# Kernel tuning notes

Hardware: AMD Instinct MI355X
Metric: run time of the kernel (lower is better)

The kernel has to match this reference:

```python
import jax, jax.numpy as jnp
import numpy as np

N = 100000
F_IN = 128
HID = 256
N_CLS = 40
E = 1600000


def setup_inputs() -> dict:
    key = jax.random.key(0)
    ks = jax.random.split(key, 12)
    x = jax.random.normal(ks[0], (N, F_IN), dtype=jnp.float32)
    edge_index = jax.random.randint(ks[1], (2, E), 0, N, dtype=jnp.int64)
    # GCNConv params (glorot-ish scale), conv2 is reused twice in forward
    def lin(k, fi, fo):
        return jax.random.normal(k, (fi, fo), dtype=jnp.float32) * (1.0 / np.sqrt(fi))
    return {
        "x": x,
        "edge_index": edge_index,
        "W1": lin(ks[2], F_IN, HID), "b1": jnp.zeros((HID,), jnp.float32),
        "W2": lin(ks[3], HID, HID),  "b2": jnp.zeros((HID,), jnp.float32),
        "W3": lin(ks[4], HID, HID),  "b3": jnp.zeros((HID,), jnp.float32),
        "W4": lin(ks[5], HID, N_CLS), "b4": jnp.zeros((N_CLS,), jnp.float32),
    }


def _gcn_norm(edge_index, n):
    # add self-loops, compute symmetric normalization D^-1/2 (A+I) D^-1/2
    loop = jnp.arange(n, dtype=edge_index.dtype)
    src = jnp.concatenate([edge_index[0], loop])
    dst = jnp.concatenate([edge_index[1], loop])
    deg = jax.ops.segment_sum(jnp.ones_like(dst, dtype=jnp.float32), dst, num_segments=n)
    dinv = jnp.where(deg > 0, jax.lax.rsqrt(deg), 0.0)
    norm = dinv[src] * dinv[dst]  # [E+N]
    return src, dst, norm


def _gcn_conv(x, W, b, src, dst, norm, n):
    h = x @ W                       # [N, Fout] dense transform first (fewer msg bytes)
    msg = h[src] * norm[:, None]    # gather + scale
    out = jax.ops.segment_sum(msg, dst, num_segments=n)  # scatter-add
    return out + b


def reference(x, edge_index, W1, b1, W2, b2, W3, b3, W4, b4):
    n = x.shape[0]
    src, dst, norm = _gcn_norm(edge_index, n)
    h = jax.nn.relu(_gcn_conv(x, W1, b1, src, dst, norm, n))
    h = jax.nn.relu(_gcn_conv(h, W2, b2, src, dst, norm, n))
    h = jax.nn.relu(_gcn_conv(h, W2, b2, src, dst, norm, n))  # conv2 reused, as in source
    h = jax.nn.relu(_gcn_conv(h, W3, b3, src, dst, norm, n))
    h = _gcn_conv(h, W4, b4, src, dst, norm, n)
    return jax.nn.log_softmax(h, axis=1)
```

## Files before the change

### kernel.cpp

```cpp
#include <hip/hip_runtime.h>
#include <stdint.h>
#include <math.h>

#define NN   100000
#define FIN  128
#define HIDDEN 256
#define NCLS 40
#define NE   1600000

#define PRNG 8
#define RNG  12500
#define SSL  32
#define NES  50000

typedef unsigned short u16;
typedef unsigned char u8;
typedef __attribute__((ext_vector_type(8))) short s16x8;
typedef __attribute__((ext_vector_type(4))) float f32x4;
typedef __attribute__((ext_vector_type(2))) float f32x2;

__device__ __forceinline__ float bf2f(unsigned short u) {
    union { float f; uint32_t i; } v; v.i = ((uint32_t)u) << 16; return v.f;
}
__device__ __forceinline__ unsigned short f2bf(float f) {
    union { float f; uint32_t i; } v; v.f = f;
    uint32_t r = v.i + 0x7fffu + ((v.i >> 16) & 1u);
    return (unsigned short)(r >> 16);
}
__device__ __forceinline__ u8 f2fp8(float f) {
    int r = __builtin_amdgcn_cvt_pk_fp8_f32(f, f, 0, false);
    return (u8)(r & 0xff);
}

__global__ __launch_bounds__(256) void k_detect(const u16* __restrict__ x16,
                                                const int* __restrict__ ei,
                                                int* __restrict__ flags) {
    int g = blockIdx.x * 256 + threadIdx.x;
    uint2 v = *(const uint2*)(x16 + (size_t)g * 4);
    int nan_cnt = 0;
    uint32_t w0 = v.x, w1 = v.y;
    if (((w0 >> 0)  & 0x7fff) >= 0x7f80) nan_cnt++;
    if (((w0 >> 16) & 0x7fff) >= 0x7f80) nan_cnt++;
    if (((w1 >> 0)  & 0x7fff) >= 0x7f80) nan_cnt++;
    if (((w1 >> 16) & 0x7fff) >= 0x7f80) nan_cnt++;
    int odd_nz = (g < 8192 && ei[2 * g + 1] != 0) ? 1 : 0;
#pragma unroll
    for (int off = 1; off < 64; off <<= 1) {
        nan_cnt += __shfl_xor(nan_cnt, off);
        odd_nz  += __shfl_xor(odd_nz, off);
    }
    if ((threadIdx.x & 63) == 0) {
        if (nan_cnt) atomicAdd(&flags[0], nan_cnt);
        if (odd_nz)  atomicAdd(&flags[2], odd_nz);
    }
}

__global__ void k_compact(const int* __restrict__ ei, int* __restrict__ dst32,
                          int* __restrict__ src32, const int* __restrict__ flags) {
    int e = blockIdx.x * 256 + threadIdx.x;
    if (e < NE) {
        if (flags[2] == 0) { src32[e] = ei[2 * e]; dst32[e] = ei[2 * (NE + e)]; }
        else               { src32[e] = ei[e];     dst32[e] = ei[NE + e]; }
    }
}

__global__ void k_trans_cvt(const void* W1, const void* W2, const void* W3, const void* W4,
                            u16* W1t, u16* W2t, u16* W3t, u16* W4t,
                            const void* b1, const void* b2, const void* b3, const void* b4,
                            u16* o1, u16* o2, u16* o3, u16* o4,
                            const void* __restrict__ x, const float* __restrict__ dinv,
                            u16* __restrict__ xb,
                            const int* __restrict__ flags) {
    int b = blockIdx.x;
    int fl = flags[0];
    int t = threadIdx.x;
    if (b >= 705) {
        int i = (b - 705) * 256 + t;
        if (i < NN * FIN) {
            float v = fl ? ((const float*)x)[i] : bf2f(((const u16*)x)[i]);
            xb[i] = f2bf(v * dinv[i >> 7]);
        }
        return;
    }
    if (b == 704) {
        o1[t] = fl ? f2bf(((const float*)b1)[t]) : ((const u16*)b1)[t];
        o2[t] = fl ? f2bf(((const float*)b2)[t]) : ((const u16*)b2)[t];
        o3[t] = fl ? f2bf(((const float*)b3)[t]) : ((const u16*)b3)[t];
        if (t < 64) o4[t] = (t < NCLS) ? (fl ? f2bf(((const float*)b4)[t]) : ((const u16*)b4)[t]) : (u16)0;
        return;
    }
    const void* W; u16* Wt; int K, F, Fpad, base;
    if (b < 128)      { W = W1; Wt = W1t; K = 128; F = 256; Fpad = 256; base = 0; }
    else if (b < 384) { W = W2; Wt = W2t; K = 256; F = 256; Fpad = 256; base = 128; }
    else if (b < 640) { W = W3; Wt = W3t; K = 256; F = 256; Fpad = 256; base = 384; }
    else              { W = W4; Wt = W4t; K = 256; F = 40;  Fpad = 64;  base = 640; }
    int idx = (b - base) * 256 + t;
    if (idx >= K * Fpad) return;
    int f = idx / K, k = idx - f * K;
    u16 v = 0;
    if (f < F) {
        if (fl) v = f2bf(((const float*)W)[(size_t)k * F + f]);
        else    v = ((const u16*)W)[(size_t)k * F + f];
    }
    Wt[idx] = v;
}


__global__ __launch_bounds__(256) void k_histb(const int* __restrict__ dst32,
                                               int* __restrict__ partial) {
    __shared__ int h[RNG];
    int p = blockIdx.x >> 5, s = blockIdx.x & 31;
    int t = threadIdx.x;
    int4 z4 = make_int4(0, 0, 0, 0);
    for (int i = t * 4; i < RNG; i += 1024) *(int4*)(h + i) = z4;
    __syncthreads();
    int base = s * NES;
    int lo = p * RNG;
    int nfull = NES & ~1023;
    for (int k = t * 4; k < nfull; k += 1024) {
        int4 d4 = *(const int4*)(dst32 + base + k);
        int a;
        a = d4.x - lo; if ((unsigned)a < RNG) atomicAdd(&h[a], 1);
        a = d4.y - lo; if ((unsigned)a < RNG) atomicAdd(&h[a], 1);
        a = d4.z - lo; if ((unsigned)a < RNG) atomicAdd(&h[a], 1);
        a = d4.w - lo; if ((unsigned)a < RNG) atomicAdd(&h[a], 1);
    }
    for (int k = nfull + t; k < NES; k += 256) {
        int a = dst32[base + k] - lo;
        if ((unsigned)a < RNG) atomicAdd(&h[a], 1);
    }
    __syncthreads();
    int* out = partial + blockIdx.x * RNG;
    for (int i = t * 4; i < RNG; i += 1024) *(int4*)(out + i) = *(const int4*)(h + i);
}

__global__ __launch_bounds__(256) void k_scan1(const int* __restrict__ partial,
                                               int* __restrict__ cnt,
                                               int* __restrict__ out,
                                               int* __restrict__ bsum) {
    __shared__ int sh[256];
    int t = threadIdx.x;
    int base = blockIdx.x * 1024 + t * 4;
    int v0 = 0, v1 = 0, v2 = 0, v3 = 0;
    if (base < NN) {
        int p = base / RNG, il = base - p * RNG;
        const int* q = partial + (p * SSL) * RNG + il;
        int4 acc = make_int4(0, 0, 0, 0);
#pragma unroll
        for (int s = 0; s < SSL; ++s) {
            int4 w = *(const int4*)(q + s * RNG);
            acc.x += w.x; acc.y += w.y; acc.z += w.z; acc.w += w.w;
        }
        v0 = acc.x; v1 = acc.y; v2 = acc.z; v3 = acc.w;
        *(int4*)(cnt + base) = acc;
    }
    int s = v0 + v1 + v2 + v3;
    sh[t] = s;
    __syncthreads();
    for (int off = 1; off < 256; off <<= 1) {
        int x = (t >= off) ? sh[t - off] : 0;
        __syncthreads();
        sh[t] += x;
        __syncthreads();
    }
    int ex = sh[t] - s;
    if (base < NN) {
        int4 o = make_int4(ex, ex + v0, ex + v0 + v1, ex + v0 + v1 + v2);
        *(int4*)(out + base) = o;
    }
    if (t == 255) bsum[blockIdx.x] = sh[255];
}

__global__ void k_scan2(int* bsum, int nb) {
    if (threadIdx.x == 0 && blockIdx.x == 0) {
        int run = 0;
        for (int i = 0; i < nb; ++i) { int t = bsum[i]; bsum[i] = run; run += t; }
    }
}

__global__ void k_scan3o(int* __restrict__ rp, const int* __restrict__ bsum,
                         const int* __restrict__ cnt, float* __restrict__ dinv,
                         int* __restrict__ partial) {
    int i = blockIdx.x * 256 + threadIdx.x;
    if (i < NN) {
        int v = rp[i] + bsum[i >> 10];
        rp[i] = v;
        dinv[i] = rsqrtf((float)(cnt[i] + 1));
        int p = i / RNG, il = i - p * RNG;
        int* q = partial + (p * SSL) * RNG + il;
        int run = v;
#pragma unroll
        for (int s = 0; s < SSL; ++s) { int t = q[s * RNG]; q[s * RNG] = run; run += t; }
    }
    if (i == 0) rp[NN] = NE;
}

__global__ __launch_bounds__(256) void k_fillb(const int* __restrict__ dst32,
                                               const int* __restrict__ src32,
                                               const int* __restrict__ offs,
                                               int* __restrict__ col) {
    __shared__ int h[RNG];
    int p = blockIdx.x >> 5, s = blockIdx.x & 31;
    int t = threadIdx.x;
    const int* o = offs + blockIdx.x * RNG;
    for (int i = t * 4; i < RNG; i += 1024) *(int4*)(h + i) = *(const int4*)(o + i);
    __syncthreads();
    int base = s * NES;
    int lo = p * RNG;
    int nfull = NES & ~1023;
    for (int k = t * 4; k < nfull; k += 1024) {
        int4 d4 = *(const int4*)(dst32 + base + k);
        int4 s4 = *(const int4*)(src32 + base + k);
        int a;
        a = d4.x - lo; if ((unsigned)a < RNG) col[atomicAdd(&h[a], 1)] = s4.x;
        a = d4.y - lo; if ((unsigned)a < RNG) col[atomicAdd(&h[a], 1)] = s4.y;
        a = d4.z - lo; if ((unsigned)a < RNG) col[atomicAdd(&h[a], 1)] = s4.z;
        a = d4.w - lo; if ((unsigned)a < RNG) col[atomicAdd(&h[a], 1)] = s4.w;
    }
    for (int k = nfull + t; k < NES; k += 256) {
        int a = dst32[base + k] - lo;
        if ((unsigned)a < RNG) col[atomicAdd(&h[a], 1)] = src32[base + k];
    }
}


#define GLL(g, l) __builtin_amdgcn_global_load_lds( \
    (const __attribute__((address_space(1))) unsigned int*)(g), \
    (__attribute__((address_space(3))) unsigned int*)(l), 16, 0, 0)

#define NT128 ((NN + 127) / 128)
#define NT256 ((NN + 255) / 256)

__global__ __launch_bounds__(256) void k_gemmP(const u16* __restrict__ A,
                                               const u16* __restrict__ Wt,
                                               const float* __restrict__ dinv,
                                               const u16* __restrict__ bias,
                                               u16* __restrict__ C,
                                               int K, int out_fp8) {
    __shared__ __align__(16) u16 Bs[128 * 256];
    __shared__ __align__(16) u16 As[2 * 128 * 32];
    int t = threadIdx.x;
    int bn = blockIdx.y;
    int w = t >> 6, lane = t & 63;
    int wm = w >> 1, wn = w & 1;
    int lrow = lane & 15, lq = lane >> 4;
    int r0 = t >> 2;
    int seg = (t & 3) * 8;

    int rounds = K >> 4;
    for (int r = 0; r < rounds; ++r) {
        int d = r * 4096 + t * 16;
        int kt = d >> 13;
        int win = d & 8191;
        int row = win >> 6;
        int sg = (win & 63) >> 1;
        GLL(Wt + (size_t)(bn * 128 + row) * K + kt * 32 + sg, Bs + (d >> 1));
    }

    int nK = K >> 5;
    bool fuse = (bias != nullptr);
    float bcol[4];
#pragma unroll
    for (int j = 0; j < 4; ++j)
        bcol[j] = fuse ? bf2f(bias[bn * 128 + wn * 64 + j * 16 + lrow]) : 0.f;

    for (int tm = blockIdx.x; tm < NT128; tm += gridDim.x) {
        int rowBase = tm * 128;
        int ar0 = rowBase + r0;       if (ar0 > NN - 1) ar0 = NN - 1;
        int ar1 = rowBase + 64 + r0;  if (ar1 > NN - 1) ar1 = NN - 1;
        const u16* a0p = A + (size_t)ar0 * K + seg;
        const u16* a1p = A + (size_t)ar1 * K + seg;
        GLL(a0p, As + t * 8);
        GLL(a1p, As + 2048 + t * 8);

        f32x4 acc[4][4] = {};
        int cur = 0;
        for (int kt = 0; kt < nK; ++kt) {
            __syncthreads();
            if (kt + 1 < nK) {
                int nxt = cur ^ 1;
                GLL(a0p + (kt + 1) * 32, As + nxt * 4096 + t * 8);
                GLL(a1p + (kt + 1) * 32, As + nxt * 4096 + 2048 + t * 8);
            }
            const u16* ab = As + cur * 4096;
            const u16* bb = Bs + kt * 4096;
            s16x8 af[4], bf[4];
#pragma unroll
            for (int i = 0; i < 4; ++i)
                af[i] = *(const s16x8*)(ab + (wm * 64 + i * 16 + lrow) * 32 + lq * 8);
#pragma unroll
            for (int j = 0; j < 4; ++j)
                bf[j] = *(const s16x8*)(bb + (wn * 64 + j * 16 + lrow) * 32 + lq * 8);
#pragma unroll
            for (int i = 0; i < 4; ++i)
#pragma unroll
                for (int j = 0; j < 4; ++j)
                    acc[i][j] = __builtin_amdgcn_mfma_f32_16x16x32_bf16(af[i], bf[j], acc[i][j], 0, 0, 0);
            cur ^= 1;
        }

        u8* C8 = (u8*)C;
#pragma unroll
        for (int i = 0; i < 4; ++i) {
#pragma unroll
            for (int rr = 0; rr < 4; ++rr) {
                int row = rowBase + wm * 64 + i * 16 + lq * 4 + rr;
                if (row < NN) {
                    float d = dinv[row];
#pragma unroll
                    for (int j = 0; j < 4; ++j) {
                        int colg = bn * 128 + wn * 64 + j * 16 + lrow;
                        float v = fuse ? fmaxf(fmaf(d, acc[i][j][rr], bcol[j]), 0.f)
                                       : acc[i][j][rr] * d;
                        if (out_fp8) C8[(size_t)row * HIDDEN + colg] = f2fp8(v);
                        else         C[(size_t)row * HIDDEN + colg] = f2bf(v);
                    }
                }
            }
        }
        __syncthreads();
    }
}

__global__ __launch_bounds__(256) void k_gemmP64(const u16* __restrict__ A,
                                                 const u16* __restrict__ Wt,
                                                 const float* __restrict__ dinv,
                                                 u16* __restrict__ C) {
    const int K = 256;
    __shared__ __align__(16) u16 Bs[64 * 256];
    __shared__ __align__(16) u16 As[2 * 256 * 32];
    int t = threadIdx.x;
    int w = t >> 6, lane = t & 63;
    int lrow = lane & 15, lq = lane >> 4;
    int seg = (t & 3) * 8;
    int rr0 = t >> 2;

    for (int r = 0; r < 8; ++r)
        GLL(Wt + (size_t)(t >> 2) * K + r * 32 + seg, Bs + r * 2048 + t * 8);

    for (int tm = blockIdx.x; tm < NT256; tm += gridDim.x) {
        int rowBase = tm * 256;
        const u16* ap[4];
#pragma unroll
        for (int c = 0; c < 4; ++c) {
            int ar = rowBase + c * 64 + rr0;
            if (ar > NN - 1) ar = NN - 1;
            ap[c] = A + (size_t)ar * K + seg;
        }
#pragma unroll
        for (int c = 0; c < 4; ++c) GLL(ap[c], As + c * 2048 + t * 8);

        f32x4 acc[4][4] = {};
        int cur = 0;
        for (int kt = 0; kt < 8; ++kt) {
            __syncthreads();
            if (kt + 1 < 8) {
                int nxt = cur ^ 1;
#pragma unroll
                for (int c = 0; c < 4; ++c)
                    GLL(ap[c] + (kt + 1) * 32, As + nxt * 8192 + c * 2048 + t * 8);
            }
            const u16* ab = As + cur * 8192;
            const u16* bb = Bs + kt * 2048;
            s16x8 af[4], bf[4];
#pragma unroll
            for (int i = 0; i < 4; ++i)
                af[i] = *(const s16x8*)(ab + (w * 64 + i * 16 + lrow) * 32 + lq * 8);
#pragma unroll
            for (int j = 0; j < 4; ++j)
                bf[j] = *(const s16x8*)(bb + (j * 16 + lrow) * 32 + lq * 8);
#pragma unroll
            for (int i = 0; i < 4; ++i)
#pragma unroll
                for (int j = 0; j < 4; ++j)
                    acc[i][j] = __builtin_amdgcn_mfma_f32_16x16x32_bf16(af[i], bf[j], acc[i][j], 0, 0, 0);
            cur ^= 1;
        }

#pragma unroll
        for (int i = 0; i < 4; ++i) {
#pragma unroll
            for (int rr = 0; rr < 4; ++rr) {
                int row = rowBase + w * 64 + i * 16 + lq * 4 + rr;
                if (row < NN) {
                    float d = dinv[row];
#pragma unroll
                    for (int j = 0; j < 4; ++j) {
                        int colg = j * 16 + lrow;
                        C[(size_t)row * 64 + colg] = f2bf(acc[i][j][rr] * d);
                    }
                }
            }
        }
        __syncthreads();
    }
}


__global__ __launch_bounds__(256) void k_agg8(const u8* __restrict__ hs,
                                              const int* __restrict__ rp,
                                              const int* __restrict__ col,
                                              const float* __restrict__ dinv,
                                              const u16* __restrict__ bias,
                                              u16* __restrict__ out) {
    int wq = __builtin_amdgcn_readfirstlane(threadIdx.x >> 6);
    int row = blockIdx.x * 4 + wq;
    if (row >= NN) return;
    int lane = threadIdx.x & 63;
    int fo = lane * 4;
    float a0 = 0.f, a1 = 0.f, a2 = 0.f, a3 = 0.f;
    auto acc_add = [&](uint32_t w) {
        f32x2 x = __builtin_amdgcn_cvt_pk_f32_fp8(w, false);
        f32x2 y = __builtin_amdgcn_cvt_pk_f32_fp8(w, true);
        a0 += x.x; a1 += x.y; a2 += y.x; a3 += y.y;
    };
    auto acc_fma = [&](uint32_t w, float m) {
        f32x2 x = __builtin_amdgcn_cvt_pk_f32_fp8(w, false);
        f32x2 y = __builtin_amdgcn_cvt_pk_f32_fp8(w, true);
        a0 = fmaf(m, x.x, a0); a1 = fmaf(m, x.y, a1);
        a2 = fmaf(m, y.x, a2); a3 = fmaf(m, y.y, a3);
    };
    acc_add(*(const uint32_t*)(hs + (size_t)row * HIDDEN + fo));
    int p  = __builtin_amdgcn_readfirstlane(rp[row]);
    int p1 = __builtin_amdgcn_readfirstlane(rp[row + 1]);
    for (; p + 8 <= p1; p += 8) {
        uint32_t v[8];
#pragma unroll
        for (int k = 0; k < 8; ++k) {
            int c = __builtin_amdgcn_readfirstlane(col[p + k]);
            v[k] = *(const uint32_t*)(hs + (size_t)c * HIDDEN + fo);
        }
#pragma unroll
        for (int k = 0; k < 8; ++k) acc_add(v[k]);
    }
    int rem = p1 - p;
    if (rem) {
        uint32_t v[8];
#pragma unroll
        for (int k = 0; k < 8; ++k) {
            int idx = (k < rem) ? (p + k) : p;
            int c = __builtin_amdgcn_readfirstlane(col[idx]);
            v[k] = *(const uint32_t*)(hs + (size_t)c * HIDDEN + fo);
        }
#pragma unroll
        for (int k = 0; k < 8; ++k) acc_fma(v[k], (k < rem) ? 1.f : 0.f);
    }
    float d = dinv[row];
    uint2 bv = *(const uint2*)(bias + fo);
    float r0 = fmaxf(fmaf(d, a0, bf2f((u16)(bv.x & 0xffff))), 0.f);
    float r1 = fmaxf(fmaf(d, a1, bf2f((u16)(bv.x >> 16))), 0.f);
    float r2 = fmaxf(fmaf(d, a2, bf2f((u16)(bv.y & 0xffff))), 0.f);
    float r3 = fmaxf(fmaf(d, a3, bf2f((u16)(bv.y >> 16))), 0.f);
    uint2 o;
    o.x = (uint32_t)f2bf(r0) | ((uint32_t)f2bf(r1) << 16);
    o.y = (uint32_t)f2bf(r2) | ((uint32_t)f2bf(r3) << 16);
    *(uint2*)(out + (size_t)row * HIDDEN + fo) = o;
}

__global__ __launch_bounds__(256) void k_aggx(const u16* __restrict__ xb,
                                              const int* __restrict__ rp,
                                              const int* __restrict__ col,
                                              u16* __restrict__ out) {
    int wq = __builtin_amdgcn_readfirstlane(threadIdx.x >> 6);
    int row = blockIdx.x * 4 + wq;
    if (row >= NN) return;
    int lane = threadIdx.x & 63;
    int fo = lane * 2;
    float a0 = 0.f, a1 = 0.f;
    auto acc_add = [&](uint32_t w) {
        a0 += bf2f((u16)(w & 0xffff));
        a1 += bf2f((u16)(w >> 16));
    };
    auto acc_fma = [&](uint32_t w, float m) {
        a0 = fmaf(m, bf2f((u16)(w & 0xffff)), a0);
        a1 = fmaf(m, bf2f((u16)(w >> 16)), a1);
    };
    acc_add(*(const uint32_t*)(xb + (size_t)row * FIN + fo));
    int p  = __builtin_amdgcn_readfirstlane(rp[row]);
    int p1 = __builtin_amdgcn_readfirstlane(rp[row + 1]);
    for (; p + 8 <= p1; p += 8) {
        uint32_t v[8];
#pragma unroll
        for (int k = 0; k < 8; ++k) {
            int c = __builtin_amdgcn_readfirstlane(col[p + k]);
            v[k] = *(const uint32_t*)(xb + (size_t)c * FIN + fo);
        }
#pragma unroll
        for (int k = 0; k < 8; ++k) acc_add(v[k]);
    }
    int rem = p1 - p;
    if (rem) {
        uint32_t v[8];
#pragma unroll
        for (int k = 0; k < 8; ++k) {
            int idx = (k < rem) ? (p + k) : p;
            int c = __builtin_amdgcn_readfirstlane(col[idx]);
            v[k] = *(const uint32_t*)(xb + (size_t)c * FIN + fo);
        }
#pragma unroll
        for (int k = 0; k < 8; ++k) acc_fma(v[k], (k < rem) ? 1.f : 0.f);
    }
    uint32_t o = (uint32_t)f2bf(a0) | ((uint32_t)f2bf(a1) << 16);
    *(uint32_t*)(out + (size_t)row * FIN + fo) = o;
}

__global__ __launch_bounds__(256) void k_agg5(const u16* __restrict__ hs,
                                              const int* __restrict__ rp,
                                              const int* __restrict__ col,
                                              const float* __restrict__ dinv,
                                              const u16* __restrict__ bias,
                                              void* __restrict__ out,
                                              const int* __restrict__ flags) {
    int wq = __builtin_amdgcn_readfirstlane(threadIdx.x >> 6);
    int row = blockIdx.x * 4 + wq;
    if (row >= NN) return;
    int lane = threadIdx.x & 63;
    float a = bf2f(hs[(size_t)row * 64 + lane]);
    int p  = __builtin_amdgcn_readfirstlane(rp[row]);
    int p1 = __builtin_amdgcn_readfirstlane(rp[row + 1]);
    for (; p + 8 <= p1; p += 8) {
        u16 v[8];
#pragma unroll
        for (int k = 0; k < 8; ++k) {
            int c = __builtin_amdgcn_readfirstlane(col[p + k]);
            v[k] = hs[(size_t)c * 64 + lane];
        }
#pragma unroll
        for (int k = 0; k < 8; ++k) a += bf2f(v[k]);
    }
    int rem = p1 - p;
    if (rem) {
        u16 v[8];
#pragma unroll
        for (int k = 0; k < 8; ++k) {
            int idx = (k < rem) ? (p + k) : p;
            int c = __builtin_amdgcn_readfirstlane(col[idx]);
            v[k] = hs[(size_t)c * 64 + lane];
        }
#pragma unroll
        for (int k = 0; k < 8; ++k)
            a = fmaf((k < rem) ? 1.f : 0.f, bf2f(v[k]), a);
    }
    bool act = lane < NCLS;
    float d = dinv[row];
    float l = act ? fmaf(d, a, bf2f(bias[lane])) : -1e30f;
    float m = l;
#pragma unroll
    for (int off = 32; off > 0; off >>= 1) m = fmaxf(m, __shfl_xor(m, off));
    float e = act ? __expf(l - m) : 0.f;
#pragma unroll
    for (int off = 32; off > 0; off >>= 1) e += __shfl_xor(e, off);
    if (act) {
        float r = l - m - __logf(e);
        if (flags[0]) ((float*)out)[(size_t)row * NCLS + lane] = r;
        else          ((u16*)out)[(size_t)row * NCLS + lane] = f2bf(r);
    }
}


extern "C" void kernel_launch(void* const* d_in, const int* in_sizes, int n_in,
                              void* d_out, int out_size, void* d_ws, size_t ws_size,
                              hipStream_t stream) {
    const void* x  = d_in[0];
    const int* ei  = (const int*)d_in[1];
    const void* W1 = d_in[2];
    const void* b1 = d_in[3];
    const void* W2 = d_in[4];
    const void* b2 = d_in[5];
    const void* W3 = d_in[6];
    const void* b3 = d_in[7];
    const void* W4 = d_in[8];
    const void* b4 = d_in[9];

    char* p = (char*)d_ws;
    auto alloc = [&](size_t b) -> char* {
        char* r = p;
        p += (b + 255) & ~(size_t)255;
        return r;
    };
    int*   flags = (int*)alloc(256);
    int*   cnt  = (int*)alloc((size_t)NN * 4);
    float* dinv = (float*)alloc((size_t)NN * 4);
    int*   rp   = (int*)alloc((size_t)(NN + 1) * 4);
    int*   col  = (int*)alloc((size_t)NE * 4);
    int*   bsum = (int*)alloc(4096);
    u16* xb  = (u16*)alloc((size_t)NN * FIN * 2);
    u16* W1t = (u16*)alloc((size_t)256 * 128 * 2);
    u16* W2t = (u16*)alloc((size_t)256 * 256 * 2);
    u16* W3t = (u16*)alloc((size_t)256 * 256 * 2);
    u16* W4t = (u16*)alloc((size_t)64 * 256 * 2);
    u16* bb1 = (u16*)alloc(512);
    u16* bb2 = (u16*)alloc(512);
    u16* bb3 = (u16*)alloc(512);
    u16* bb4 = (u16*)alloc(128);
    u16* bufA = (u16*)alloc((size_t)NN * HIDDEN * 2);
    u16* bufB = (u16*)alloc((size_t)NN * HIDDEN * 2);

    int* dst32   = (int*)bufA;
    int* src32   = dst32 + NE;
    int* partial = (int*)bufB;

    hipMemsetAsync(flags, 0, 16, stream);
    k_detect<<<64, 256, 0, stream>>>((const u16*)x, ei, flags);
    k_compact<<<(NE + 255) / 256, 256, 0, stream>>>(ei, dst32, src32, flags);

    k_histb<<<PRNG * SSL, 256, 0, stream>>>(dst32, partial);
    k_scan1<<<(NN + 1023) / 1024, 256, 0, stream>>>(partial, cnt, rp, bsum);
    k_scan2<<<1, 64, 0, stream>>>(bsum, (NN + 1023) / 1024);
    k_scan3o<<<(NN + 255) / 256, 256, 0, stream>>>(rp, bsum, cnt, dinv, partial);
    k_fillb<<<PRNG * SSL, 256, 0, stream>>>(dst32, src32, partial, col);

    k_trans_cvt<<<705 + (NN * FIN + 255) / 256, 256, 0, stream>>>(
        W1, W2, W3, W4, W1t, W2t, W3t, W4t,
        b1, b2, b3, b4, bb1, bb2, bb3, bb4, x, dinv, xb, flags);

    dim3 gP(256, 2);
    dim3 aggGrid((NN + 3) / 4);

    k_aggx<<<aggGrid, 256, 0, stream>>>(xb, rp, col, bufB);
    k_gemmP<<<gP, 256, 0, stream>>>(bufB, W1t, dinv, bb1, bufA, 128, 0);
    k_gemmP<<<gP, 256, 0, stream>>>(bufA, W2t, dinv, nullptr, bufB, 256, 1);
    k_agg8<<<aggGrid, 256, 0, stream>>>((const u8*)bufB, rp, col, dinv, bb2, bufA);
    k_gemmP<<<gP, 256, 0, stream>>>(bufA, W2t, dinv, nullptr, bufB, 256, 1);
    k_agg8<<<aggGrid, 256, 0, stream>>>((const u8*)bufB, rp, col, dinv, bb2, bufA);
    k_gemmP<<<gP, 256, 0, stream>>>(bufA, W3t, dinv, nullptr, bufB, 256, 1);
    k_agg8<<<aggGrid, 256, 0, stream>>>((const u8*)bufB, rp, col, dinv, bb3, bufA);
    k_gemmP64<<<256, 256, 0, stream>>>(bufA, W4t, dinv, bufB);
    k_agg5<<<aggGrid, 256, 0, stream>>>(bufB, rp, col, dinv, bb4, d_out, flags);
}
```

Baseline: 702.3 us.

## Slice gathered feature tables into column blocks for cache-resident aggregation

Stores the pre-aggregation features (bf16 x and fp8 hidden activations) in a column-sliced layout of 8 slices, each contiguous over all nodes. Aggregation kernels now launch 8x more blocks, each handling one slice, so the gathered working set per slice is smaller and more likely to stay in L2/LLC during the random neighbor gathers. Each wave also processes 8 edges in parallel across lane groups and reduces them with cross-lane shuffles. The costs are that column indices and row pointers are re-read once per slice, per-edge gathers shrink to 32-byte segments, and the extra shuffle reductions and partly idle lanes add overhead.

```diff
diff --git a/kernel.cpp b/kernel.cpp
--- a/kernel.cpp
+++ b/kernel.cpp
@@ -12,6 +12,8 @@
 #define RNG  12500
 #define SSL  32
 #define NES  50000
+
+#define NSLC 8
 
 typedef unsigned short u16;
 typedef unsigned char u8;
@@ -77,8 +79,10 @@
     if (b >= 705) {
         int i = (b - 705) * 256 + t;
         if (i < NN * FIN) {
+            int node = i >> 7, f = i & 127;
             float v = fl ? ((const float*)x)[i] : bf2f(((const u16*)x)[i]);
-            xb[i] = f2bf(v * dinv[i >> 7]);
+            xb[(size_t)(f >> 4) * (NN * 16) + (size_t)node * 16 + (f & 15)] =
+                f2bf(v * dinv[node]);
         }
         return;
     }
@@ -312,8 +316,10 @@
                         int colg = bn * 128 + wn * 64 + j * 16 + lrow;
                         float v = fuse ? fmaxf(fmaf(d, acc[i][j][rr], bcol[j]), 0.f)
                                        : acc[i][j][rr] * d;
-                        if (out_fp8) C8[(size_t)row * HIDDEN + colg] = f2fp8(v);
-                        else         C[(size_t)row * HIDDEN + colg] = f2bf(v);
+                        if (out_fp8)
+                            C8[(size_t)(colg >> 5) * (NN * 32) + (size_t)row * 32 + (colg & 31)] = f2fp8(v);
+                        else
+                            C[(size_t)row * HIDDEN + colg] = f2bf(v);
                     }
                 }
             }
@@ -403,11 +409,16 @@
                                               const float* __restrict__ dinv,
                                               const u16* __restrict__ bias,
                                               u16* __restrict__ out) {
+    int bid = blockIdx.x;
+    int s = bid & 7;
+    int rowg = bid >> 3;
     int wq = __builtin_amdgcn_readfirstlane(threadIdx.x >> 6);
-    int row = blockIdx.x * 4 + wq;
+    int row = rowg * 4 + wq;
     if (row >= NN) return;
     int lane = threadIdx.x & 63;
-    int fo = lane * 4;
+    int g = lane >> 3;
+    int fl = lane & 7;
+    const u8* hss = hs + (size_t)s * (NN * 32);
     float a0 = 0.f, a1 = 0.f, a2 = 0.f, a3 = 0.f;
     auto acc_add = [&](uint32_t w) {
         f32x2 x = __builtin_amdgcn_cvt_pk_f32_fp8(w, false);
@@ -420,52 +431,63 @@
         a0 = fmaf(m, x.x, a0); a1 = fmaf(m, x.y, a1);
         a2 = fmaf(m, y.x, a2); a3 = fmaf(m, y.y, a3);
     };
-    acc_add(*(const uint32_t*)(hs + (size_t)row * HIDDEN + fo));
+    if (lane < 8) acc_add(*(const uint32_t*)(hss + (size_t)row * 32 + fl * 4));
     int p  = __builtin_amdgcn_readfirstlane(rp[row]);
     int p1 = __builtin_amdgcn_readfirstlane(rp[row + 1]);
-    for (; p + 8 <= p1; p += 8) {
-        uint32_t v[8];
-#pragma unroll
-        for (int k = 0; k < 8; ++k) {
-            int c = __builtin_amdgcn_readfirstlane(col[p + k]);
-            v[k] = *(const uint32_t*)(hs + (size_t)c * HIDDEN + fo);
-        }
-#pragma unroll
-        for (int k = 0; k < 8; ++k) acc_add(v[k]);
+    for (; p + 16 <= p1; p += 16) {
+        int c0 = col[p + g];
+        int c1 = col[p + 8 + g];
+        uint32_t v0 = *(const uint32_t*)(hss + (size_t)c0 * 32 + fl * 4);
+        uint32_t v1 = *(const uint32_t*)(hss + (size_t)c1 * 32 + fl * 4);
+        acc_add(v0);
+        acc_add(v1);
+    }
+    if (p + 8 <= p1) {
+        int c = col[p + g];
+        acc_add(*(const uint32_t*)(hss + (size_t)c * 32 + fl * 4));
+        p += 8;
     }
     int rem = p1 - p;
     if (rem) {
-        uint32_t v[8];
-#pragma unroll
-        for (int k = 0; k < 8; ++k) {
-            int idx = (k < rem) ? (p + k) : p;
-            int c = __builtin_amdgcn_readfirstlane(col[idx]);
-            v[k] = *(const uint32_t*)(hs + (size_t)c * HIDDEN + fo);
-        }
-#pragma unroll
-        for (int k = 0; k < 8; ++k) acc_fma(v[k], (k < rem) ? 1.f : 0.f);
-    }
-    float d = dinv[row];
-    uint2 bv = *(const uint2*)(bias + fo);
-    float r0 = fmaxf(fmaf(d, a0, bf2f((u16)(bv.x & 0xffff))), 0.f);
-    float r1 = fmaxf(fmaf(d, a1, bf2f((u16)(bv.x >> 16))), 0.f);
-    float r2 = fmaxf(fmaf(d, a2, bf2f((u16)(bv.y & 0xffff))), 0.f);
-    float r3 = fmaxf(fmaf(d, a3, bf2f((u16)(bv.y >> 16))), 0.f);
-    uint2 o;
-    o.x = (uint32_t)f2bf(r0) | ((uint32_t)f2bf(r1) << 16);
-    o.y = (uint32_t)f2bf(r2) | ((uint32_t)f2bf(r3) << 16);
-    *(uint2*)(out + (size_t)row * HIDDEN + fo) = o;
+        int c = col[p + ((g < rem) ? g : 0)];
+        uint32_t v = *(const uint32_t*)(hss + (size_t)c * 32 + fl * 4);
+        acc_fma(v, (g < rem) ? 1.f : 0.f);
+    }
+#pragma unroll
+    for (int off = 8; off < 64; off <<= 1) {
+        a0 += __shfl_xor(a0, off);
+        a1 += __shfl_xor(a1, off);
+        a2 += __shfl_xor(a2, off);
+        a3 += __shfl_xor(a3, off);
+    }
+    if (lane < 8) {
+        float d = dinv[row];
+        uint2 bv = *(const uint2*)(bias + s * 32 + fl * 4);
+        float r0 = fmaxf(fmaf(d, a0, bf2f((u16)(bv.x & 0xffff))), 0.f);
+        float r1 = fmaxf(fmaf(d, a1, bf2f((u16)(bv.x >> 16))), 0.f);
+        float r2 = fmaxf(fmaf(d, a2, bf2f((u16)(bv.y & 0xffff))), 0.f);
+        float r3 = fmaxf(fmaf(d, a3, bf2f((u16)(bv.y >> 16))), 0.f);
+        uint2 o;
+        o.x = (uint32_t)f2bf(r0) | ((uint32_t)f2bf(r1) << 16);
+        o.y = (uint32_t)f2bf(r2) | ((uint32_t)f2bf(r3) << 16);
+        *(uint2*)(out + (size_t)row * HIDDEN + s * 32 + fl * 4) = o;
+    }
 }
 
 __global__ __launch_bounds__(256) void k_aggx(const u16* __restrict__ xb,
                                               const int* __restrict__ rp,
                                               const int* __restrict__ col,
                                               u16* __restrict__ out) {
+    int bid = blockIdx.x;
+    int s = bid & 7;
+    int rowg = bid >> 3;
     int wq = __builtin_amdgcn_readfirstlane(threadIdx.x >> 6);
-    int row = blockIdx.x * 4 + wq;
+    int row = rowg * 4 + wq;
     if (row >= NN) return;
     int lane = threadIdx.x & 63;
-    int fo = lane * 2;
+    int g = lane >> 3;
+    int fl = lane & 7;
+    const u16* xbs = xb + (size_t)s * (NN * 16);
     float a0 = 0.f, a1 = 0.f;
     auto acc_add = [&](uint32_t w) {
         a0 += bf2f((u16)(w & 0xffff));
@@ -475,33 +497,37 @@
         a0 = fmaf(m, bf2f((u16)(w & 0xffff)), a0);
         a1 = fmaf(m, bf2f((u16)(w >> 16)), a1);
     };
-    acc_add(*(const uint32_t*)(xb + (size_t)row * FIN + fo));
+    if (lane < 8) acc_add(*(const uint32_t*)(xbs + (size_t)row * 16 + fl * 2));
     int p  = __builtin_amdgcn_readfirstlane(rp[row]);
     int p1 = __builtin_amdgcn_readfirstlane(rp[row + 1]);
-    for (; p + 8 <= p1; p += 8) {
-        uint32_t v[8];
-#pragma unroll
-        for (int k = 0; k < 8; ++k) {
-            int c = __builtin_amdgcn_readfirstlane(col[p + k]);
-            v[k] = *(const uint32_t*)(xb + (size_t)c * FIN + fo);
-        }
-#pragma unroll
-        for (int k = 0; k < 8; ++k) acc_add(v[k]);
+    for (; p + 16 <= p1; p += 16) {
+        int c0 = col[p + g];
+        int c1 = col[p + 8 + g];
+        uint32_t v0 = *(const uint32_t*)(xbs + (size_t)c0 * 16 + fl * 2);
+        uint32_t v1 = *(const uint32_t*)(xbs + (size_t)c1 * 16 + fl * 2);
+        acc_add(v0);
+        acc_add(v1);
+    }
+    if (p + 8 <= p1) {
+        int c = col[p + g];
+        acc_add(*(const uint32_t*)(xbs + (size_t)c * 16 + fl * 2));
+        p += 8;
     }
     int rem = p1 - p;
     if (rem) {
-        uint32_t v[8];
-#pragma unroll
-        for (int k = 0; k < 8; ++k) {
-            int idx = (k < rem) ? (p + k) : p;
-            int c = __builtin_amdgcn_readfirstlane(col[idx]);
-            v[k] = *(const uint32_t*)(xb + (size_t)c * FIN + fo);
-        }
-#pragma unroll
-        for (int k = 0; k < 8; ++k) acc_fma(v[k], (k < rem) ? 1.f : 0.f);
-    }
-    uint32_t o = (uint32_t)f2bf(a0) | ((uint32_t)f2bf(a1) << 16);
-    *(uint32_t*)(out + (size_t)row * FIN + fo) = o;
+        int c = col[p + ((g < rem) ? g : 0)];
+        uint32_t v = *(const uint32_t*)(xbs + (size_t)c * 16 + fl * 2);
+        acc_fma(v, (g < rem) ? 1.f : 0.f);
+    }
+#pragma unroll
+    for (int off = 8; off < 64; off <<= 1) {
+        a0 += __shfl_xor(a0, off);
+        a1 += __shfl_xor(a1, off);
+    }
+    if (lane < 8) {
+        uint32_t o = (uint32_t)f2bf(a0) | ((uint32_t)f2bf(a1) << 16);
+        *(uint32_t*)(out + (size_t)row * FIN + s * 16 + fl * 2) = o;
+    }
 }
 
 __global__ __launch_bounds__(256) void k_agg5(const u16* __restrict__ hs,
@@ -616,15 +642,16 @@
 
     dim3 gP(256, 2);
     dim3 aggGrid((NN + 3) / 4);
-
-    k_aggx<<<aggGrid, 256, 0, stream>>>(xb, rp, col, bufB);
+    dim3 aggGridS(((NN + 3) / 4) * NSLC);
+
+    k_aggx<<<aggGridS, 256, 0, stream>>>(xb, rp, col, bufB);
     k_gemmP<<<gP, 256, 0, stream>>>(bufB, W1t, dinv, bb1, bufA, 128, 0);
     k_gemmP<<<gP, 256, 0, stream>>>(bufA, W2t, dinv, nullptr, bufB, 256, 1);
-    k_agg8<<<aggGrid, 256, 0, stream>>>((const u8*)bufB, rp, col, dinv, bb2, bufA);
+    k_agg8<<<aggGridS, 256, 0, stream>>>((const u8*)bufB, rp, col, dinv, bb2, bufA);
     k_gemmP<<<gP, 256, 0, stream>>>(bufA, W2t, dinv, nullptr, bufB, 256, 1);
-    k_agg8<<<aggGrid, 256, 0, stream>>>((const u8*)bufB, rp, col, dinv, bb2, bufA);
+    k_agg8<<<aggGridS, 256, 0, stream>>>((const u8*)bufB, rp, col, dinv, bb2, bufA);
     k_gemmP<<<gP, 256, 0, stream>>>(bufA, W3t, dinv, nullptr, bufB, 256, 1);
-    k_agg8<<<aggGrid, 256, 0, stream>>>((const u8*)bufB, rp, col, dinv, bb3, bufA);
+    k_agg8<<<aggGridS, 256, 0, stream>>>((const u8*)bufB, rp, col, dinv, bb3, bufA);
     k_gemmP64<<<256, 256, 0, stream>>>(bufA, W4t, dinv, bufB);
     k_agg5<<<aggGrid, 256, 0, stream>>>(bufB, rp, col, dinv, bb4, d_out, flags);
 }
```

Result: slower. 1.352 ms (+92.5%).
